# Kernel optimization log

Hardware: AMD Instinct MI355X
Metric: run time of the kernel (lower is better)

## Reference

```python
import jax, jax.numpy as jnp
import numpy as np

N, E = 50000, 800000            # nodes, edges
IN_F, HID, HEADS, NCLS = 128, 32, 8, 40
NEG_SLOPE = 0.2                 # DGL GATConv default


def setup_inputs() -> dict:
    key = jax.random.key(0)
    ks = jax.random.split(key, 11)
    glorot = lambda k, shape, fan: jax.random.normal(k, shape, jnp.float32) * (1.0 / np.sqrt(fan))
    return {
        "x": jax.random.normal(ks[0], (N, IN_F), jnp.float32),
        "src": jax.random.randint(ks[1], (E,), 0, N, jnp.int32),
        "dst": jax.random.randint(ks[2], (E,), 0, N, jnp.int32),
        # layer 1: GATConv(IN_F -> HID, 8 heads, elu)
        "W1": glorot(ks[3], (IN_F, HEADS * HID), IN_F),
        "al1": glorot(ks[4], (HEADS, HID), HID),
        "ar1": glorot(ks[5], (HEADS, HID), HID),
        "b1": jnp.zeros((HEADS * HID,), jnp.float32),
        # layer 2: GATConv(HEADS*HID -> NCLS, 1 head, no activation)
        "W2": glorot(ks[6], (HEADS * HID, NCLS), HEADS * HID),
        "al2": glorot(ks[7], (1, NCLS), NCLS),
        "ar2": glorot(ks[8], (1, NCLS), NCLS),
        "b2": jnp.zeros((NCLS,), jnp.float32),
    }


def gat_layer(x, W, al, ar, b, src, dst, n_nodes, apply_elu):
    """DGL GATConv: fc -> per-edge leaky_relu attention -> edge softmax -> scatter-sum."""
    H, D = al.shape
    h = (x @ W).reshape(-1, H, D)                     # [N, H, D]
    el = jnp.einsum('nhd,hd->nh', h, al)              # [N, H]
    er = jnp.einsum('nhd,hd->nh', h, ar)              # [N, H]
    e = jax.nn.leaky_relu(el[src] + er[dst], NEG_SLOPE)   # [E, H]
    # segment softmax over incoming edges of each dst node
    m = jax.lax.stop_gradient(jax.ops.segment_max(e, dst, num_segments=n_nodes))
    ex = jnp.exp(e - m[dst])
    denom = jax.ops.segment_sum(ex, dst, num_segments=n_nodes)
    alpha = ex / jnp.maximum(denom[dst], 1e-9)        # [E, H]
    out = jax.ops.segment_sum(h[src] * alpha[:, :, None], dst, num_segments=n_nodes)
    out = out + b.reshape(H, D)
    if apply_elu:
        out = jax.nn.elu(out)
    return out.reshape(n_nodes, H * D)                # flatten(1)


def reference(x, src, dst, W1, al1, ar1, b1, W2, al2, ar2, b2):
    n = x.shape[0]
    h = gat_layer(x, W1, al1, ar1, b1, src, dst, n, True)
    return gat_layer(h, W2, al2, ar2, b2, src, dst, n, False)
```

## Files before the change

### kernel.cpp

```cpp
#include <hip/hip_runtime.h>
#include <hip/hip_bf16.h>
#include <math.h>

#define NNODES 50000
#define NEDGES 800000
#define INF    128
#define HIDD   32
#define HEADS  8
#define C1     256
#define NCLS   40
#define NCP    48

typedef unsigned int  uint;
typedef unsigned short ushort;
typedef __attribute__((ext_vector_type(8))) short short8v;
typedef __attribute__((ext_vector_type(4))) float f32x4;

__device__ __forceinline__ float bf2f(ushort v) {
  return __uint_as_float(((uint)v) << 16);
}
__device__ __forceinline__ ushort f2bf(float f) {
  __hip_bfloat16 b = __float2bfloat16(f);
  return *reinterpret_cast<ushort*>(&b);
}
__device__ __forceinline__ float ldv(const void* p, long i, int isf) {
  return isf ? ((const float*)p)[i] : bf2f(((const ushort*)p)[i]);
}
__device__ __forceinline__ uint packbf2(float f0, float f1) {
  return (uint)f2bf(f0) | ((uint)f2bf(f1) << 16);
}
__device__ __forceinline__ float lrelu(float x) {
  return (x >= 0.f) ? x : 0.2f * x;
}

__global__ __launch_bounds__(256) void k_init(const ushort* __restrict__ xr,
                                              int* __restrict__ flag,
                                              int* __restrict__ deg) {
  const int g = blockIdx.x * 256 + threadIdx.x;
  if (g < NNODES) deg[g] = 0;
  if (blockIdx.x == 0 && threadIdx.x < 64) {
    const int t = threadIdx.x;
    int c = 0;
    for (int i = t; i < 4096; i += 64) {
      const uint e = (xr[i] >> 7) & 0xFFu;
      if (e > 200u) c++;
    }
#pragma unroll
    for (int k = 32; k >= 1; k >>= 1) c += __shfl_xor(c, k, 64);
    if (t == 0) flag[0] = (c > 100) ? 1 : 0;
  }
}

__global__ void k_hist(const int* __restrict__ dst, int* __restrict__ deg,
                       int* __restrict__ erank) {
  const int e = (blockIdx.x * 256 + threadIdx.x) << 2;
  if (e < NEDGES) {
    const int4 d4 = *reinterpret_cast<const int4*>(dst + e);
    int4 r4;
    r4.x = atomicAdd(&deg[d4.x], 1);
    r4.y = atomicAdd(&deg[d4.y], 1);
    r4.z = atomicAdd(&deg[d4.z], 1);
    r4.w = atomicAdd(&deg[d4.w], 1);
    *reinterpret_cast<int4*>(erank + e) = r4;
  }
}

__global__ __launch_bounds__(1024) void k_scan1(const int* __restrict__ deg,
                                                int* __restrict__ rowptr,
                                                int* __restrict__ bsum) {
  __shared__ int wsum[16];
  const int t = threadIdx.x;
  const int i = blockIdx.x * 1024 + t;
  const int lane = t & 63, wv = t >> 6;
  const int v = (i < NNODES) ? deg[i] : 0;
  int p = v;
#pragma unroll
  for (int off = 1; off < 64; off <<= 1) {
    int u = __shfl_up(p, off, 64);
    if (lane >= off) p += u;
  }
  if (lane == 63) wsum[wv] = p;
  __syncthreads();
  if (wv == 0) {
    int s = (lane < 16) ? wsum[lane] : 0;
#pragma unroll
    for (int off = 1; off < 16; off <<= 1) {
      int u = __shfl_up(s, off, 64);
      if (lane >= off) s += u;
    }
    if (lane < 16) wsum[lane] = s;
  }
  __syncthreads();
  const int wbase = (wv > 0) ? wsum[wv - 1] : 0;
  if (i < NNODES) rowptr[i] = wbase + p - v;
  if (t == 1023) bsum[blockIdx.x] = wbase + p;
}

__global__ __launch_bounds__(1024) void k_scan3(int* __restrict__ rowptr,
                                                const int* __restrict__ bsum,
                                                int nb) {
  __shared__ int base_s;
  const int t = threadIdx.x;
  if (t < 64) {
    const int v = (t < nb) ? bsum[t] : 0;
    int p = v;
#pragma unroll
    for (int off = 1; off < 64; off <<= 1) {
      int u = __shfl_up(p, off, 64);
      if (t >= off) p += u;
    }
    if (t == (int)blockIdx.x) base_s = p - v;
  }
  __syncthreads();
  const int i = blockIdx.x * 1024 + t;
  if (i < NNODES) rowptr[i] += base_s;
}

__global__ void k_scatter(const int* __restrict__ src, const int* __restrict__ dst,
                          const int* __restrict__ rowptr,
                          const int* __restrict__ erank,
                          int* __restrict__ colsrc) {
  const int e = (blockIdx.x * 256 + threadIdx.x) << 2;
  if (e < NEDGES) {
    const int4 s4 = *reinterpret_cast<const int4*>(src + e);
    const int4 d4 = *reinterpret_cast<const int4*>(dst + e);
    const int4 r4 = *reinterpret_cast<const int4*>(erank + e);
    colsrc[rowptr[d4.x] + r4.x] = s4.x;
    colsrc[rowptr[d4.y] + r4.y] = s4.y;
    colsrc[rowptr[d4.z] + r4.z] = s4.z;
    colsrc[rowptr[d4.w] + r4.w] = s4.w;
  }
}

__global__ __launch_bounds__(256) void k_prep(const void* __restrict__ W1r,
                                              const void* __restrict__ W2r,
                                              const int* __restrict__ flag,
                                              ushort* __restrict__ w1tb,
                                              ushort* __restrict__ w2tb) {
  const int b = blockIdx.x;
  const int isf = flag[0];
  if (b < INF) {
    const int k = b, n = threadIdx.x;
    w1tb[(size_t)n * INF + k] = f2bf(ldv(W1r, (long)k * C1 + n, isf));
  } else {
    const int n = b - INF, k = threadIdx.x;
    w2tb[(size_t)n * C1 + k] =
        (n < NCLS) ? f2bf(ldv(W2r, (long)k * NCLS + n, isf)) : (ushort)0;
  }
}

__global__ __launch_bounds__(256) void k_gemm1m(const void* __restrict__ Xr,
                                                const ushort* __restrict__ w1tb,
                                                const void* __restrict__ alr,
                                                const void* __restrict__ arr,
                                                const int* __restrict__ flag,
                                                ushort* __restrict__ Hb,
                                                float* __restrict__ el,
                                                float* __restrict__ er) {
  __shared__ __align__(16) ushort xs[32 * 136];
  const int tid = threadIdx.x;
  const int rt  = blockIdx.x * 32;
  const int isf = flag[0];

  {
    const int r  = tid >> 4;
    const int c0 = (tid & 15) << 3;
#pragma unroll
    for (int p = 0; p < 2; ++p) {
      const int row  = r + (p << 4);
      const int grow = rt + row;
      uint4 u = make_uint4(0u, 0u, 0u, 0u);
      if (grow < NNODES) {
        if (isf) {
          const float* Xf = (const float*)Xr;
          const float4 a = *reinterpret_cast<const float4*>(Xf + (size_t)grow * INF + c0);
          const float4 b = *reinterpret_cast<const float4*>(Xf + (size_t)grow * INF + c0 + 4);
          u.x = packbf2(a.x, a.y);
          u.y = packbf2(a.z, a.w);
          u.z = packbf2(b.x, b.y);
          u.w = packbf2(b.z, b.w);
        } else {
          const ushort* Xb = (const ushort*)Xr;
          u = *reinterpret_cast<const uint4*>(Xb + (size_t)grow * INF + c0);
        }
      }
      *reinterpret_cast<uint4*>(&xs[row * 136 + c0]) = u;
    }
  }
  __syncthreads();

  const int lane = tid & 63;
  const int wv   = tid >> 6;
  const int n0   = wv << 6;
  const int col  = lane & 15;
  const int quad = lane >> 4;

  short8v bf[16];
#pragma unroll
  for (int ct = 0; ct < 4; ++ct)
#pragma unroll
    for (int ks = 0; ks < 4; ++ks)
      bf[ct * 4 + ks] = *reinterpret_cast<const short8v*>(
          &w1tb[(size_t)(n0 + ct * 16 + col) * INF + (ks << 5) + (quad << 3)]);
  short8v af[8];
#pragma unroll
  for (int rt2 = 0; rt2 < 2; ++rt2)
#pragma unroll
    for (int ks = 0; ks < 4; ++ks)
      af[rt2 * 4 + ks] = *reinterpret_cast<const short8v*>(
          &xs[(rt2 * 16 + col) * 136 + (ks << 5) + (quad << 3)]);

  f32x4 acc[8];
#pragma unroll
  for (int i = 0; i < 8; ++i) acc[i] = (f32x4){0.f, 0.f, 0.f, 0.f};

#pragma unroll
  for (int rt2 = 0; rt2 < 2; ++rt2)
#pragma unroll
    for (int ct = 0; ct < 4; ++ct)
#pragma unroll
      for (int ks = 0; ks < 4; ++ks)
        acc[rt2 * 4 + ct] = __builtin_amdgcn_mfma_f32_16x16x32_bf16(
            af[rt2 * 4 + ks], bf[ct * 4 + ks], acc[rt2 * 4 + ct], 0, 0, 0);

#pragma unroll
  for (int rt2 = 0; rt2 < 2; ++rt2)
#pragma unroll
    for (int ct = 0; ct < 4; ++ct)
#pragma unroll
      for (int r = 0; r < 4; ++r) {
        const int row = rt + rt2 * 16 + (quad << 2) + r;
        if (row < NNODES)
          Hb[(size_t)row * C1 + n0 + (ct << 4) + col] = f2bf(acc[rt2 * 4 + ct][r]);
      }

  float alv[4], arv[4];
#pragma unroll
  for (int ct = 0; ct < 4; ++ct) {
    alv[ct] = ldv(alr, n0 + ct * 16 + col, isf);
    arv[ct] = ldv(arr, n0 + ct * 16 + col, isf);
  }
#pragma unroll
  for (int rt2 = 0; rt2 < 2; ++rt2)
#pragma unroll
    for (int r = 0; r < 4; ++r) {
      float pl0 = acc[rt2 * 4 + 0][r] * alv[0] + acc[rt2 * 4 + 1][r] * alv[1];
      float pl1 = acc[rt2 * 4 + 2][r] * alv[2] + acc[rt2 * 4 + 3][r] * alv[3];
      float pr0 = acc[rt2 * 4 + 0][r] * arv[0] + acc[rt2 * 4 + 1][r] * arv[1];
      float pr1 = acc[rt2 * 4 + 2][r] * arv[2] + acc[rt2 * 4 + 3][r] * arv[3];
#pragma unroll
      for (int k = 1; k <= 8; k <<= 1) {
        pl0 += __shfl_xor(pl0, k, 64);
        pl1 += __shfl_xor(pl1, k, 64);
        pr0 += __shfl_xor(pr0, k, 64);
        pr1 += __shfl_xor(pr1, k, 64);
      }
      if (col == 0) {
        const int row = rt + rt2 * 16 + (quad << 2) + r;
        if (row < NNODES) {
          el[row * HEADS + 2 * wv]     = pl0;
          el[row * HEADS + 2 * wv + 1] = pl1;
          er[row * HEADS + 2 * wv]     = pr0;
          er[row * HEADS + 2 * wv + 1] = pr1;
        }
      }
    }
}

__global__ __launch_bounds__(256) void k_agg1(const int* __restrict__ rowptr,
                                              const int* __restrict__ deg,
                                              const int* __restrict__ colsrc,
                                              const float* __restrict__ el,
                                              const float* __restrict__ er,
                                              const ushort* __restrict__ h1b,
                                              const void* __restrict__ b1r,
                                              const int* __restrict__ flag,
                                              ushort* __restrict__ out1b) {
  const int n = blockIdx.x * 4 + (threadIdx.x >> 6);
  if (n >= NNODES) return;
  const int t  = threadIdx.x & 63;
  const int c0 = t << 2;
  const int h  = t >> 3;
  const int isf = flag[0];
  const int start = rowptr[n];
  const int cnt   = deg[n];
  const char* hp  = (const char*)h1b;
  const char* elp = (const char*)el;
  const float ern = er[n * HEADS + h];
  const int* cp = colsrc + start;
  const uint cb = (uint)c0 << 1;
  const uint hb = (uint)h << 2;
  float a0 = 0.f, a1 = 0.f, a2 = 0.f, a3 = 0.f, den = 0.f;
  int i = 0;
  for (; i + 8 <= cnt; i += 8) {
    int s[8];
#pragma unroll
    for (int j = 0; j < 8; ++j) s[j] = cp[i + j];
    float l[8];
#pragma unroll
    for (int j = 0; j < 8; ++j)
      l[j] = *reinterpret_cast<const float*>(elp + (((uint)s[j] << 5) | hb));
    uint2 u[8];
#pragma unroll
    for (int j = 0; j < 8; ++j)
      u[j] = *reinterpret_cast<const uint2*>(hp + (((uint)s[j] << 9) | cb));
#pragma unroll
    for (int j = 0; j < 8; ++j) {
      const float e = __expf(lrelu(l[j] + ern));
      den += e;
      a0 += e * __uint_as_float(u[j].x << 16);
      a1 += e * __uint_as_float(u[j].x & 0xffff0000u);
      a2 += e * __uint_as_float(u[j].y << 16);
      a3 += e * __uint_as_float(u[j].y & 0xffff0000u);
    }
  }
  for (; i < cnt; ++i) {
    const int s = cp[i];
    const float l = *reinterpret_cast<const float*>(elp + (((uint)s << 5) | hb));
    const uint2 u = *reinterpret_cast<const uint2*>(hp + (((uint)s << 9) | cb));
    const float e = __expf(lrelu(l + ern));
    den += e;
    a0 += e * __uint_as_float(u.x << 16);
    a1 += e * __uint_as_float(u.x & 0xffff0000u);
    a2 += e * __uint_as_float(u.y << 16);
    a3 += e * __uint_as_float(u.y & 0xffff0000u);
  }
  const float inv = 1.f / fmaxf(den, 1e-9f);
  float o0 = a0 * inv + ldv(b1r, c0 + 0, isf);
  float o1 = a1 * inv + ldv(b1r, c0 + 1, isf);
  float o2 = a2 * inv + ldv(b1r, c0 + 2, isf);
  float o3 = a3 * inv + ldv(b1r, c0 + 3, isf);
  o0 = (o0 > 0.f) ? o0 : expm1f(o0);
  o1 = (o1 > 0.f) ? o1 : expm1f(o1);
  o2 = (o2 > 0.f) ? o2 : expm1f(o2);
  o3 = (o3 > 0.f) ? o3 : expm1f(o3);
  uint2 w;
  w.x = packbf2(o0, o1);
  w.y = packbf2(o2, o3);
  *reinterpret_cast<uint2*>((char*)out1b + ((uint)n << 9) + cb) = w;
}

__global__ __launch_bounds__(256) void k_gemm2m(const ushort* __restrict__ Ab,
                                                const ushort* __restrict__ w2tb,
                                                const void* __restrict__ alr,
                                                const void* __restrict__ arr,
                                                const int* __restrict__ flag,
                                                ushort* __restrict__ Hb,
                                                float* __restrict__ el,
                                                float* __restrict__ er) {
  __shared__ __align__(16) ushort as2[64 * 264];
  const int tid = threadIdx.x;
  const int rt  = blockIdx.x * 64;
  const int isf = flag[0];

  {
    const int r  = tid >> 2;
    const int cb = (tid & 3) << 6;
    const int grow = rt + r;
#pragma unroll
    for (int j = 0; j < 8; ++j) {
      uint4 u = make_uint4(0u, 0u, 0u, 0u);
      if (grow < NNODES)
        u = *reinterpret_cast<const uint4*>(Ab + (size_t)grow * C1 + cb + (j << 3));
      *reinterpret_cast<uint4*>(&as2[r * 264 + cb + (j << 3)]) = u;
    }
  }
  __syncthreads();

  const int lane = tid & 63;
  const int wv   = tid >> 6;
  const int col  = lane & 15;
  const int quad = lane >> 4;

  f32x4 acc[3];
#pragma unroll
  for (int i = 0; i < 3; ++i) acc[i] = (f32x4){0.f, 0.f, 0.f, 0.f};

#pragma unroll
  for (int ks = 0; ks < 8; ++ks) {
    const int k0 = (ks << 5) + (quad << 3);
    const short8v a = *reinterpret_cast<const short8v*>(&as2[(wv * 16 + col) * 264 + k0]);
    const short8v b0 = *reinterpret_cast<const short8v*>(&w2tb[(size_t)( 0 + col) * C1 + k0]);
    const short8v b1 = *reinterpret_cast<const short8v*>(&w2tb[(size_t)(16 + col) * C1 + k0]);
    const short8v b2 = *reinterpret_cast<const short8v*>(&w2tb[(size_t)(32 + col) * C1 + k0]);
    acc[0] = __builtin_amdgcn_mfma_f32_16x16x32_bf16(a, b0, acc[0], 0, 0, 0);
    acc[1] = __builtin_amdgcn_mfma_f32_16x16x32_bf16(a, b1, acc[1], 0, 0, 0);
    acc[2] = __builtin_amdgcn_mfma_f32_16x16x32_bf16(a, b2, acc[2], 0, 0, 0);
  }

  float alv[3], arv[3];
#pragma unroll
  for (int ct = 0; ct < 3; ++ct) {
    const int gc = ct * 16 + col;
    alv[ct] = (gc < NCLS) ? ldv(alr, gc, isf) : 0.f;
    arv[ct] = (gc < NCLS) ? ldv(arr, gc, isf) : 0.f;
  }
#pragma unroll
  for (int r = 0; r < 4; ++r) {
    const int row = rt + wv * 16 + (quad << 2) + r;
    const bool rok = row < NNODES;
#pragma unroll
    for (int ct = 0; ct < 3; ++ct) {
      const int gc = ct * 16 + col;
      if (rok && gc < NCLS)
        Hb[(size_t)row * NCLS + gc] = f2bf(acc[ct][r]);
    }
    float pl = acc[0][r] * alv[0] + acc[1][r] * alv[1] + acc[2][r] * alv[2];
    float pr = acc[0][r] * arv[0] + acc[1][r] * arv[1] + acc[2][r] * arv[2];
#pragma unroll
    for (int k = 1; k <= 8; k <<= 1) {
      pl += __shfl_xor(pl, k, 64);
      pr += __shfl_xor(pr, k, 64);
    }
    if (col == 0 && rok) {
      el[row] = pl;
      er[row] = pr;
    }
  }
}

__global__ __launch_bounds__(256) void k_agg2(const int* __restrict__ rowptr,
                                              const int* __restrict__ deg,
                                              const int* __restrict__ colsrc,
                                              const float* __restrict__ el,
                                              const float* __restrict__ er,
                                              const ushort* __restrict__ h2b,
                                              const void* __restrict__ b2r,
                                              const int* __restrict__ flag,
                                              float* __restrict__ out) {
  const int t    = threadIdx.x;
  const int lane = t & 63;
  const int n    = blockIdx.x * 4 + (t >> 6);
  if (n >= NNODES) return;
  const int isf  = flag[0];
  const int start = rowptr[n];
  const int cnt   = deg[n];
  const float ern = er[n];
  const bool act = lane < NCLS;
  const char* hp = (const char*)h2b;
  const uint lb = (uint)lane << 1;
  const int* cp = colsrc + start;
  float acc = 0.f, den = 0.f;
  int i = 0;
  for (; i + 8 <= cnt; i += 8) {
    int s[8];
#pragma unroll
    for (int j = 0; j < 8; ++j) s[j] = cp[i + j];
    float l[8];
#pragma unroll
    for (int j = 0; j < 8; ++j) l[j] = el[s[j]];
    float v[8];
#pragma unroll
    for (int j = 0; j < 8; ++j)
      v[j] = act ? bf2f(*reinterpret_cast<const ushort*>(hp + (uint)s[j] * 80u + lb)) : 0.f;
#pragma unroll
    for (int j = 0; j < 8; ++j) {
      const float e = __expf(lrelu(l[j] + ern));
      den += e;
      acc += e * v[j];
    }
  }
  for (; i < cnt; ++i) {
    const int s = cp[i];
    const float ex = __expf(lrelu(el[s] + ern));
    den += ex;
    if (act) acc += ex * bf2f(*reinterpret_cast<const ushort*>(hp + (uint)s * 80u + lb));
  }
  if (act) {
    const float o = acc / fmaxf(den, 1e-9f) + ldv(b2r, lane, isf);
    out[(size_t)n * NCLS + lane] = o;
  }
}

extern "C" void kernel_launch(void* const* d_in, const int* in_sizes, int n_in,
                              void* d_out, int out_size, void* d_ws, size_t ws_size,
                              hipStream_t stream) {
  int ix = -1, iW1 = -1, iW2 = -1, e1 = -1, e2 = -1;
  int i256[3] = {-1, -1, -1}, n256 = 0;
  int i40[3]  = {-1, -1, -1}, n40 = 0;
  for (int i = 0; i < n_in; ++i) {
    switch (in_sizes[i]) {
      case 6400000: ix = i; break;
      case 800000:  if (e1 < 0) e1 = i; else e2 = i; break;
      case 32768:   iW1 = i; break;
      case 10240:   iW2 = i; break;
      case 256:     if (n256 < 3) i256[n256++] = i; break;
      case 40:      if (n40 < 3)  i40[n40++]  = i; break;
      default: break;
    }
  }
  bool mapped = (ix >= 0 && iW1 >= 0 && iW2 >= 0 && e2 >= 0 && n256 == 3 && n40 == 3);
  int isrc, idst;
  if (mapped) {
    const bool dict_order = (in_sizes[0] == 6400000);
    isrc = dict_order ? e1 : e2;
    idst = dict_order ? e2 : e1;
  } else {
    ix = 0; isrc = 1; idst = 2; iW1 = 3;
    i256[0] = 4; i256[1] = 5; i256[2] = 6;
    iW2 = 7; i40[0] = 8; i40[1] = 9; i40[2] = 10;
  }
  const void* X   = d_in[ix];
  const int*  src = (const int*)d_in[isrc];
  const int*  dst = (const int*)d_in[idst];
  const void* W1  = d_in[iW1];
  const void* al1 = d_in[i256[0]];
  const void* ar1 = d_in[i256[1]];
  const void* b1  = d_in[i256[2]];
  const void* W2  = d_in[iW2];
  const void* al2 = d_in[i40[0]];
  const void* ar2 = d_in[i40[1]];
  const void* b2  = d_in[i40[2]];

  char* ws = (char*)d_ws;
  size_t off = 0;
  auto alloc = [&](size_t bytes) -> void* {
    void* p = ws + off;
    off = (off + bytes + 255) & ~(size_t)255;
    return p;
  };
  int*    flag   = (int*)alloc(256);
  int*    deg    = (int*)alloc((size_t)NNODES * 4);
  int*    rowptr = (int*)alloc((size_t)NNODES * 4);
  int*    bsum   = (int*)alloc(256 * 4);
  int*    erank  = (int*)alloc((size_t)NEDGES * 4);
  int*    colsrc = (int*)alloc((size_t)NEDGES * 4);
  float*  el1    = (float*)alloc((size_t)NNODES * HEADS * 4);
  float*  er1    = (float*)alloc((size_t)NNODES * HEADS * 4);
  float*  el2    = (float*)alloc((size_t)NNODES * 4);
  float*  er2    = (float*)alloc((size_t)NNODES * 4);
  ushort* w1tb   = (ushort*)alloc((size_t)C1 * INF * 2);
  ushort* w2tb   = (ushort*)alloc((size_t)NCP * C1 * 2);
  ushort* h1b    = (ushort*)alloc((size_t)NNODES * C1 * 2);
  ushort* out1b  = (ushort*)alloc((size_t)NNODES * C1 * 2);
  ushort* h2b    = (ushort*)alloc((size_t)NNODES * NCLS * 2);

  const int NSB = (NNODES + 1023) / 1024;

  k_init<<<(NNODES + 255) / 256, 256, 0, stream>>>((const ushort*)X, flag, deg);
  k_hist<<<(NEDGES / 4 + 255) / 256, 256, 0, stream>>>(dst, deg, erank);
  k_scan1<<<NSB, 1024, 0, stream>>>(deg, rowptr, bsum);
  k_scan3<<<NSB, 1024, 0, stream>>>(rowptr, bsum, NSB);
  k_scatter<<<(NEDGES / 4 + 255) / 256, 256, 0, stream>>>(src, dst, rowptr, erank, colsrc);

  k_prep<<<INF + NCP, 256, 0, stream>>>(W1, W2, flag, w1tb, w2tb);

  k_gemm1m<<<(NNODES + 31) / 32, 256, 0, stream>>>(X, w1tb, al1, ar1, flag,
                                                   h1b, el1, er1);
  k_agg1<<<(NNODES + 3) / 4, 256, 0, stream>>>(rowptr, deg, colsrc, el1, er1,
                                               h1b, b1, flag, out1b);

  k_gemm2m<<<(NNODES + 63) / 64, 256, 0, stream>>>(out1b, w2tb, al2, ar2, flag,
                                                   h2b, el2, er2);
  k_agg2<<<(NNODES + 3) / 4, 256, 0, stream>>>(rowptr, deg, colsrc, el2, er2,
                                               h2b, b2, flag, (float*)d_out);
}
```

Measured before the change: 318.9 us.

## Fuse scan passes, merge scatter with weight prep, widen aggregation lanes

Replaces the two-kernel prefix scan with one kernel that uses a decoupled-lookback style flag array to get each block's base offset. It also merges the edge scatter and weight-transpose kernels into one launch. Both aggregation kernels change from 64 to 32 threads per node: layer 1 loads 8 bf16 per lane as uint4 and layer 2 loads 2 per lane as uint. This cuts launch count and wasted lanes, since 40 classes on 64 lanes left many idle. The cost is more registers per thread and a spin-wait in the scan, which relies on all 49 blocks being co-resident.

```diff
diff --git a/kernel.cpp b/kernel.cpp
--- a/kernel.cpp
+++ b/kernel.cpp
@@ -10,6 +10,8 @@
 #define C1     256
 #define NCLS   40
 #define NCP    48
+#define NSB    49
+#define SCB    ((NEDGES / 4 + 255) / 256)
 
 typedef unsigned int  uint;
 typedef unsigned short ushort;
@@ -30,14 +32,16 @@
   return (uint)f2bf(f0) | ((uint)f2bf(f1) << 16);
 }
 __device__ __forceinline__ float lrelu(float x) {
-  return (x >= 0.f) ? x : 0.2f * x;
+  return fmaxf(x, 0.2f * x);
 }
 
 __global__ __launch_bounds__(256) void k_init(const ushort* __restrict__ xr,
                                               int* __restrict__ flag,
-                                              int* __restrict__ deg) {
+                                              int* __restrict__ deg,
+                                              int* __restrict__ aggf) {
   const int g = blockIdx.x * 256 + threadIdx.x;
   if (g < NNODES) deg[g] = 0;
+  if (g < 64) aggf[g] = 0;
   if (blockIdx.x == 0 && threadIdx.x < 64) {
     const int t = threadIdx.x;
     int c = 0;
@@ -65,12 +69,13 @@
   }
 }
 
-__global__ __launch_bounds__(1024) void k_scan1(const int* __restrict__ deg,
-                                                int* __restrict__ rowptr,
-                                                int* __restrict__ bsum) {
+__global__ __launch_bounds__(1024) void k_scan(const int* __restrict__ deg,
+                                               int* __restrict__ rowptr,
+                                               int* __restrict__ aggf) {
   __shared__ int wsum[16];
-  const int t = threadIdx.x;
-  const int i = blockIdx.x * 1024 + t;
+  __shared__ int base_s;
+  const int b = blockIdx.x, t = threadIdx.x;
+  const int i = b * 1024 + t;
   const int lane = t & 63, wv = t >> 6;
   const int v = (i < NNODES) ? deg[i] : 0;
   int p = v;
@@ -91,61 +96,53 @@
     if (lane < 16) wsum[lane] = s;
   }
   __syncthreads();
+  if (t == 0) atomicExch(&aggf[b], wsum[15] + 1);
+  if (t < 64) {
+    int sum = 0;
+    for (int j = lane; j < b; j += 64) {
+      int a;
+      while ((a = atomicAdd(&aggf[j], 0)) == 0) __builtin_amdgcn_s_sleep(8);
+      sum += a - 1;
+    }
+#pragma unroll
+    for (int k = 32; k >= 1; k >>= 1) sum += __shfl_xor(sum, k, 64);
+    if (lane == 0) base_s = sum;
+  }
+  __syncthreads();
   const int wbase = (wv > 0) ? wsum[wv - 1] : 0;
-  if (i < NNODES) rowptr[i] = wbase + p - v;
-  if (t == 1023) bsum[blockIdx.x] = wbase + p;
-}
-
-__global__ __launch_bounds__(1024) void k_scan3(int* __restrict__ rowptr,
-                                                const int* __restrict__ bsum,
-                                                int nb) {
-  __shared__ int base_s;
-  const int t = threadIdx.x;
-  if (t < 64) {
-    const int v = (t < nb) ? bsum[t] : 0;
-    int p = v;
-#pragma unroll
-    for (int off = 1; off < 64; off <<= 1) {
-      int u = __shfl_up(p, off, 64);
-      if (t >= off) p += u;
-    }
-    if (t == (int)blockIdx.x) base_s = p - v;
-  }
-  __syncthreads();
-  const int i = blockIdx.x * 1024 + t;
-  if (i < NNODES) rowptr[i] += base_s;
-}
-
-__global__ void k_scatter(const int* __restrict__ src, const int* __restrict__ dst,
-                          const int* __restrict__ rowptr,
-                          const int* __restrict__ erank,
-                          int* __restrict__ colsrc) {
-  const int e = (blockIdx.x * 256 + threadIdx.x) << 2;
-  if (e < NEDGES) {
-    const int4 s4 = *reinterpret_cast<const int4*>(src + e);
-    const int4 d4 = *reinterpret_cast<const int4*>(dst + e);
-    const int4 r4 = *reinterpret_cast<const int4*>(erank + e);
-    colsrc[rowptr[d4.x] + r4.x] = s4.x;
-    colsrc[rowptr[d4.y] + r4.y] = s4.y;
-    colsrc[rowptr[d4.z] + r4.z] = s4.z;
-    colsrc[rowptr[d4.w] + r4.w] = s4.w;
-  }
-}
-
-__global__ __launch_bounds__(256) void k_prep(const void* __restrict__ W1r,
-                                              const void* __restrict__ W2r,
-                                              const int* __restrict__ flag,
-                                              ushort* __restrict__ w1tb,
-                                              ushort* __restrict__ w2tb) {
+  if (i < NNODES) rowptr[i] = base_s + wbase + p - v;
+}
+
+__global__ __launch_bounds__(256) void k_scatprep(
+    const int* __restrict__ src, const int* __restrict__ dst,
+    const int* __restrict__ rowptr, const int* __restrict__ erank,
+    int* __restrict__ colsrc,
+    const void* __restrict__ W1r, const void* __restrict__ W2r,
+    const int* __restrict__ flag,
+    ushort* __restrict__ w1tb, ushort* __restrict__ w2tb) {
   const int b = blockIdx.x;
-  const int isf = flag[0];
-  if (b < INF) {
-    const int k = b, n = threadIdx.x;
-    w1tb[(size_t)n * INF + k] = f2bf(ldv(W1r, (long)k * C1 + n, isf));
+  if (b < SCB) {
+    const int e = (b * 256 + threadIdx.x) << 2;
+    if (e < NEDGES) {
+      const int4 s4 = *reinterpret_cast<const int4*>(src + e);
+      const int4 d4 = *reinterpret_cast<const int4*>(dst + e);
+      const int4 r4 = *reinterpret_cast<const int4*>(erank + e);
+      colsrc[rowptr[d4.x] + r4.x] = s4.x;
+      colsrc[rowptr[d4.y] + r4.y] = s4.y;
+      colsrc[rowptr[d4.z] + r4.z] = s4.z;
+      colsrc[rowptr[d4.w] + r4.w] = s4.w;
+    }
   } else {
-    const int n = b - INF, k = threadIdx.x;
-    w2tb[(size_t)n * C1 + k] =
-        (n < NCLS) ? f2bf(ldv(W2r, (long)k * NCLS + n, isf)) : (ushort)0;
+    const int pb = b - SCB;
+    const int isf = flag[0];
+    if (pb < INF) {
+      const int k = pb, n = threadIdx.x;
+      w1tb[(size_t)n * INF + k] = f2bf(ldv(W1r, (long)k * C1 + n, isf));
+    } else {
+      const int n = pb - INF, k = threadIdx.x;
+      w2tb[(size_t)n * C1 + k] =
+          (n < NCLS) ? f2bf(ldv(W2r, (long)k * NCLS + n, isf)) : (ushort)0;
+    }
   }
 }
 
@@ -276,11 +273,11 @@
                                               const void* __restrict__ b1r,
                                               const int* __restrict__ flag,
                                               ushort* __restrict__ out1b) {
-  const int n = blockIdx.x * 4 + (threadIdx.x >> 6);
+  const int n = blockIdx.x * 8 + (threadIdx.x >> 5);
   if (n >= NNODES) return;
-  const int t  = threadIdx.x & 63;
-  const int c0 = t << 2;
-  const int h  = t >> 3;
+  const int t  = threadIdx.x & 31;
+  const int c0 = t << 3;
+  const int h  = t >> 2;
   const int isf = flag[0];
   const int start = rowptr[n];
   const int cnt   = deg[n];
@@ -290,54 +287,65 @@
   const int* cp = colsrc + start;
   const uint cb = (uint)c0 << 1;
   const uint hb = (uint)h << 2;
-  float a0 = 0.f, a1 = 0.f, a2 = 0.f, a3 = 0.f, den = 0.f;
+  float a[8];
+#pragma unroll
+  for (int k = 0; k < 8; ++k) a[k] = 0.f;
+  float den = 0.f;
   int i = 0;
-  for (; i + 8 <= cnt; i += 8) {
-    int s[8];
-#pragma unroll
-    for (int j = 0; j < 8; ++j) s[j] = cp[i + j];
-    float l[8];
-#pragma unroll
-    for (int j = 0; j < 8; ++j)
+  for (; i + 6 <= cnt; i += 6) {
+    int s[6];
+#pragma unroll
+    for (int j = 0; j < 6; ++j) s[j] = cp[i + j];
+    float l[6];
+#pragma unroll
+    for (int j = 0; j < 6; ++j)
       l[j] = *reinterpret_cast<const float*>(elp + (((uint)s[j] << 5) | hb));
-    uint2 u[8];
-#pragma unroll
-    for (int j = 0; j < 8; ++j)
-      u[j] = *reinterpret_cast<const uint2*>(hp + (((uint)s[j] << 9) | cb));
-#pragma unroll
-    for (int j = 0; j < 8; ++j) {
+    uint4 u[6];
+#pragma unroll
+    for (int j = 0; j < 6; ++j)
+      u[j] = *reinterpret_cast<const uint4*>(hp + (((uint)s[j] << 9) | cb));
+#pragma unroll
+    for (int j = 0; j < 6; ++j) {
       const float e = __expf(lrelu(l[j] + ern));
       den += e;
-      a0 += e * __uint_as_float(u[j].x << 16);
-      a1 += e * __uint_as_float(u[j].x & 0xffff0000u);
-      a2 += e * __uint_as_float(u[j].y << 16);
-      a3 += e * __uint_as_float(u[j].y & 0xffff0000u);
+      a[0] += e * __uint_as_float(u[j].x << 16);
+      a[1] += e * __uint_as_float(u[j].x & 0xffff0000u);
+      a[2] += e * __uint_as_float(u[j].y << 16);
+      a[3] += e * __uint_as_float(u[j].y & 0xffff0000u);
+      a[4] += e * __uint_as_float(u[j].z << 16);
+      a[5] += e * __uint_as_float(u[j].z & 0xffff0000u);
+      a[6] += e * __uint_as_float(u[j].w << 16);
+      a[7] += e * __uint_as_float(u[j].w & 0xffff0000u);
     }
   }
   for (; i < cnt; ++i) {
     const int s = cp[i];
     const float l = *reinterpret_cast<const float*>(elp + (((uint)s << 5) | hb));
-    const uint2 u = *reinterpret_cast<const uint2*>(hp + (((uint)s << 9) | cb));
+    const uint4 u = *reinterpret_cast<const uint4*>(hp + (((uint)s << 9) | cb));
     const float e = __expf(lrelu(l + ern));
     den += e;
-    a0 += e * __uint_as_float(u.x << 16);
-    a1 += e * __uint_as_float(u.x & 0xffff0000u);
-    a2 += e * __uint_as_float(u.y << 16);
-    a3 += e * __uint_as_float(u.y & 0xffff0000u);
+    a[0] += e * __uint_as_float(u.x << 16);
+    a[1] += e * __uint_as_float(u.x & 0xffff0000u);
+    a[2] += e * __uint_as_float(u.y << 16);
+    a[3] += e * __uint_as_float(u.y & 0xffff0000u);
+    a[4] += e * __uint_as_float(u.z << 16);
+    a[5] += e * __uint_as_float(u.z & 0xffff0000u);
+    a[6] += e * __uint_as_float(u.w << 16);
+    a[7] += e * __uint_as_float(u.w & 0xffff0000u);
   }
   const float inv = 1.f / fmaxf(den, 1e-9f);
-  float o0 = a0 * inv + ldv(b1r, c0 + 0, isf);
-  float o1 = a1 * inv + ldv(b1r, c0 + 1, isf);
-  float o2 = a2 * inv + ldv(b1r, c0 + 2, isf);
-  float o3 = a3 * inv + ldv(b1r, c0 + 3, isf);
-  o0 = (o0 > 0.f) ? o0 : expm1f(o0);
-  o1 = (o1 > 0.f) ? o1 : expm1f(o1);
-  o2 = (o2 > 0.f) ? o2 : expm1f(o2);
-  o3 = (o3 > 0.f) ? o3 : expm1f(o3);
-  uint2 w;
-  w.x = packbf2(o0, o1);
-  w.y = packbf2(o2, o3);
-  *reinterpret_cast<uint2*>((char*)out1b + ((uint)n << 9) + cb) = w;
+  float o[8];
+#pragma unroll
+  for (int k = 0; k < 8; ++k) {
+    float v = a[k] * inv + ldv(b1r, c0 + k, isf);
+    o[k] = (v > 0.f) ? v : expm1f(v);
+  }
+  uint4 w;
+  w.x = packbf2(o[0], o[1]);
+  w.y = packbf2(o[2], o[3]);
+  w.z = packbf2(o[4], o[5]);
+  w.w = packbf2(o[6], o[7]);
+  *reinterpret_cast<uint4*>((char*)out1b + ((uint)n << 9) + cb) = w;
 }
 
 __global__ __launch_bounds__(256) void k_gemm2m(const ushort* __restrict__ Ab,
@@ -428,19 +436,19 @@
                                               const void* __restrict__ b2r,
                                               const int* __restrict__ flag,
                                               float* __restrict__ out) {
-  const int t    = threadIdx.x;
-  const int lane = t & 63;
-  const int n    = blockIdx.x * 4 + (t >> 6);
+  const int n = blockIdx.x * 8 + (threadIdx.x >> 5);
   if (n >= NNODES) return;
+  const int t  = threadIdx.x & 31;
+  const int c0 = t << 1;
+  const bool act = c0 < NCLS;
   const int isf  = flag[0];
   const int start = rowptr[n];
   const int cnt   = deg[n];
   const float ern = er[n];
-  const bool act = lane < NCLS;
   const char* hp = (const char*)h2b;
-  const uint lb = (uint)lane << 1;
+  const uint cb = (uint)c0 << 1;
   const int* cp = colsrc + start;
-  float acc = 0.f, den = 0.f;
+  float a0 = 0.f, a1 = 0.f, den = 0.f;
   int i = 0;
   for (; i + 8 <= cnt; i += 8) {
     int s[8];
@@ -449,26 +457,32 @@
     float l[8];
 #pragma unroll
     for (int j = 0; j < 8; ++j) l[j] = el[s[j]];
-    float v[8];
+    uint u[8];
 #pragma unroll
     for (int j = 0; j < 8; ++j)
-      v[j] = act ? bf2f(*reinterpret_cast<const ushort*>(hp + (uint)s[j] * 80u + lb)) : 0.f;
+      u[j] = act ? *reinterpret_cast<const uint*>(hp + (uint)s[j] * 80u + cb) : 0u;
 #pragma unroll
     for (int j = 0; j < 8; ++j) {
       const float e = __expf(lrelu(l[j] + ern));
       den += e;
-      acc += e * v[j];
+      a0 += e * __uint_as_float(u[j] << 16);
+      a1 += e * __uint_as_float(u[j] & 0xffff0000u);
     }
   }
   for (; i < cnt; ++i) {
     const int s = cp[i];
-    const float ex = __expf(lrelu(el[s] + ern));
-    den += ex;
-    if (act) acc += ex * bf2f(*reinterpret_cast<const ushort*>(hp + (uint)s * 80u + lb));
+    const float e = __expf(lrelu(el[s] + ern));
+    den += e;
+    const uint u = act ? *reinterpret_cast<const uint*>(hp + (uint)s * 80u + cb) : 0u;
+    a0 += e * __uint_as_float(u << 16);
+    a1 += e * __uint_as_float(u & 0xffff0000u);
   }
   if (act) {
-    const float o = acc / fmaxf(den, 1e-9f) + ldv(b2r, lane, isf);
-    out[(size_t)n * NCLS + lane] = o;
+    const float inv = 1.f / fmaxf(den, 1e-9f);
+    float2 o;
+    o.x = a0 * inv + ldv(b2r, c0 + 0, isf);
+    o.y = a1 * inv + ldv(b2r, c0 + 1, isf);
+    *reinterpret_cast<float2*>(out + (size_t)n * NCLS + c0) = o;
   }
 }
 
@@ -520,9 +534,9 @@
     return p;
   };
   int*    flag   = (int*)alloc(256);
+  int*    aggf   = (int*)alloc(64 * 4);
   int*    deg    = (int*)alloc((size_t)NNODES * 4);
   int*    rowptr = (int*)alloc((size_t)NNODES * 4);
-  int*    bsum   = (int*)alloc(256 * 4);
   int*    erank  = (int*)alloc((size_t)NEDGES * 4);
   int*    colsrc = (int*)alloc((size_t)NEDGES * 4);
   float*  el1    = (float*)alloc((size_t)NNODES * HEADS * 4);
@@ -535,23 +549,19 @@
   ushort* out1b  = (ushort*)alloc((size_t)NNODES * C1 * 2);
   ushort* h2b    = (ushort*)alloc((size_t)NNODES * NCLS * 2);
 
-  const int NSB = (NNODES + 1023) / 1024;
-
-  k_init<<<(NNODES + 255) / 256, 256, 0, stream>>>((const ushort*)X, flag, deg);
+  k_init<<<(NNODES + 255) / 256, 256, 0, stream>>>((const ushort*)X, flag, deg, aggf);
   k_hist<<<(NEDGES / 4 + 255) / 256, 256, 0, stream>>>(dst, deg, erank);
-  k_scan1<<<NSB, 1024, 0, stream>>>(deg, rowptr, bsum);
-  k_scan3<<<NSB, 1024, 0, stream>>>(rowptr, bsum, NSB);
-  k_scatter<<<(NEDGES / 4 + 255) / 256, 256, 0, stream>>>(src, dst, rowptr, erank, colsrc);
-
-  k_prep<<<INF + NCP, 256, 0, stream>>>(W1, W2, flag, w1tb, w2tb);
+  k_scan<<<NSB, 1024, 0, stream>>>(deg, rowptr, aggf);
+  k_scatprep<<<SCB + INF + NCP, 256, 0, stream>>>(src, dst, rowptr, erank, colsrc,
+                                                  W1, W2, flag, w1tb, w2tb);
 
   k_gemm1m<<<(NNODES + 31) / 32, 256, 0, stream>>>(X, w1tb, al1, ar1, flag,
                                                    h1b, el1, er1);
-  k_agg1<<<(NNODES + 3) / 4, 256, 0, stream>>>(rowptr, deg, colsrc, el1, er1,
+  k_agg1<<<(NNODES + 7) / 8, 256, 0, stream>>>(rowptr, deg, colsrc, el1, er1,
                                                h1b, b1, flag, out1b);
 
   k_gemm2m<<<(NNODES + 63) / 64, 256, 0, stream>>>(out1b, w2tb, al2, ar2, flag,
                                                    h2b, el2, er2);
-  k_agg2<<<(NNODES + 3) / 4, 256, 0, stream>>>(rowptr, deg, colsrc, el2, er2,
+  k_agg2<<<(NNODES + 7) / 8, 256, 0, stream>>>(rowptr, deg, colsrc, el2, er2,
                                                h2b, b2, flag, (float*)d_out);
 }
```

Measured after the change: 293.2 us. -8.1%, faster.
